# Performance work log

Hardware: AMD Instinct MI355X
Metric: run time of the kernel (lower is better)

Reference implementation:

```python
import jax, jax.numpy as jnp
import numpy as np

S, B, IN, H, DFF, OUT, L, NHEAD, WINDOW = 2048, 4, 64, 1024, 1024, 64, 3, 4, 4
EPS = 1e-5


def _layer_norm(x, scale, bias):
    m = jnp.mean(x, axis=-1, keepdims=True)
    v = jnp.var(x, axis=-1, keepdims=True)
    return (x - m) * jax.lax.rsqrt(v + EPS) * scale + bias


def setup_inputs() -> dict:
    key = jax.random.key(0)
    ks = jax.random.split(key, 12)
    s = 0.02
    return {
        "src": jax.random.normal(ks[0], (S, B, IN), dtype=jnp.float32),
        "Wenc": jax.random.normal(ks[1], (H, IN), dtype=jnp.float32) * s,
        "benc": jnp.zeros((H,), jnp.float32),
        "Wqkv": jax.random.normal(ks[2], (L, 3 * H, H), dtype=jnp.float32) * s,
        "bqkv": jnp.zeros((L, 3 * H), jnp.float32),
        "Wo": jax.random.normal(ks[3], (L, H, H), dtype=jnp.float32) * s,
        "bo": jnp.zeros((L, H), jnp.float32),
        "W1": jax.random.normal(ks[4], (L, DFF, H), dtype=jnp.float32) * s,
        "b1": jnp.zeros((L, DFF), jnp.float32),
        "W2": jax.random.normal(ks[5], (L, H, DFF), dtype=jnp.float32) * s,
        "b2": jnp.zeros((L, H), jnp.float32),
        "ln1_s": jnp.ones((L, H), jnp.float32),
        "ln1_b": jnp.zeros((L, H), jnp.float32),
        "ln2_s": jnp.ones((L, H), jnp.float32),
        "ln2_b": jnp.zeros((L, H), jnp.float32),
        "Wout": jax.random.normal(ks[6], (OUT, H), dtype=jnp.float32) * s,
        "bout": jnp.zeros((OUT,), jnp.float32),
    }


def _banded_mask(sz):
    # triu(1) masked + lower-band (j < i-4) masked => allowed: i-4 <= j <= i
    i = jnp.arange(sz)[:, None]
    j = jnp.arange(sz)[None, :]
    allowed = (j <= i) & (j >= i - WINDOW)
    return jnp.where(allowed, 0.0, -1e9).astype(jnp.float32)


def reference(src, Wenc, benc, Wqkv, bqkv, Wo, bo, W1, b1, W2, b2,
              ln1_s, ln1_b, ln2_s, ln2_b, Wout, bout):
    dh = H // NHEAD
    mask = _banded_mask(src.shape[0])  # [S, S]
    x = src @ Wenc.T + benc  # [S, B, H]  (NOTE: pos_encoder is never applied in the source)

    def layer(x, p):
        Wqkv_, bqkv_, Wo_, bo_, W1_, b1_, W2_, b2_, s1, g1, s2, g2 = p
        qkv = x @ Wqkv_.T + bqkv_  # [S, B, 3H]
        q, k, v = jnp.split(qkv, 3, axis=-1)
        sS, sB = x.shape[0], x.shape[1]
        q = q.reshape(sS, sB, NHEAD, dh)
        k = k.reshape(sS, sB, NHEAD, dh)
        v = v.reshape(sS, sB, NHEAD, dh)
        scores = jnp.einsum('sbhd,tbhd->bhst', q, k) / jnp.sqrt(jnp.float32(dh))
        scores = scores + mask  # broadcast over [b, h]
        attn = jax.nn.softmax(scores, axis=-1)
        ctx = jnp.einsum('bhst,tbhd->sbhd', attn, v).reshape(sS, sB, H)
        attn_out = ctx @ Wo_.T + bo_
        x = _layer_norm(x + attn_out, s1, g1)  # post-norm (PyTorch default)
        ff = jax.nn.relu(x @ W1_.T + b1_) @ W2_.T + b2_
        x = _layer_norm(x + ff, s2, g2)
        return x, None

    x, _ = jax.lax.scan(layer, x, (Wqkv, bqkv, Wo, bo, W1, b1, W2, b2,
                                   ln1_s, ln1_b, ln2_s, ln2_b))
    return x @ Wout.T + bout  # [S, B, OUT]
```

## Files before the change

kernel.cpp:

```cpp
#include <hip/hip_runtime.h>
#include <hip/hip_bf16.h>

#define S_LEN   2048
#define BATCH   4
#define IN_DIM  64
#define H_DIM   1024
#define DFF_DIM 1024
#define OUT_DIM 64
#define NLAYER  3
#define NHEADS  4
#define DHEAD   256
#define WIN     4
#define ROWS    (S_LEN*BATCH)
#define QKV_LD  (3*H_DIM)


typedef __bf16 bf16x8 __attribute__((ext_vector_type(8)));
typedef float  f32x4  __attribute__((ext_vector_type(4)));

__device__ __forceinline__ float bfbits2f(unsigned int u) {
  union { unsigned int i; float f; } c; c.i = u << 16; return c.f;
}
__device__ __forceinline__ unsigned short f2bfbits(float f) {
  __hip_bfloat16 h = __float2bfloat16(f);
  return __builtin_bit_cast(unsigned short, h);
}

__device__ __forceinline__ void g2l16(const void* g, void* l) {
  __builtin_amdgcn_global_load_lds((__attribute__((address_space(1))) void*)g,
                                   (__attribute__((address_space(3))) void*)l,
                                   16, 0, 0);
}

__global__ __launch_bounds__(256)
void cvt_k(const float* __restrict__ in, __hip_bfloat16* __restrict__ out, int n)
{
  int i = (blockIdx.x * 256 + threadIdx.x) * 4;
  if (i >= n) return;
  float4 v = *(const float4*)(in + i);
  uint2 o;
  o.x = (unsigned)f2bfbits(v.x) | ((unsigned)f2bfbits(v.y) << 16);
  o.y = (unsigned)f2bfbits(v.z) | ((unsigned)f2bfbits(v.w) << 16);
  *(uint2*)(out + i) = o;
}

template<int RELU, int OUTF32>
__global__ __launch_bounds__(256, 2)
void gemm_bt(const __hip_bfloat16* __restrict__ A, int lda,
             const __hip_bfloat16* __restrict__ B,
             const float* __restrict__ bias,
             void* __restrict__ Cp, int ldc,
             int M, int N, int K)
{
  __shared__ __align__(16) __hip_bfloat16 As[128 * 32];
  __shared__ __align__(16) __hip_bfloat16 Bs[128 * 32];

  const int tid  = threadIdx.x;
  const int lane = tid & 63;
  const int wave = tid >> 6;
  const int quad = lane >> 4;
  const int l16  = lane & 15;
  const int m0 = blockIdx.y * 128;
  const int n0 = blockIdx.x * 128;
  const int wr = (wave >> 1) * 64;
  const int wc = (wave & 1) * 64;

  const int p0  = wave * 64 + lane;
  const int p1  = p0 + 256;
  const int ar0 = p0 >> 2, ac0 = (((p0 & 3) ^ ((ar0 >> 1) & 3))) * 8;
  const int ar1 = p1 >> 2, ac1 = (((p1 & 3) ^ ((ar1 >> 1) & 3))) * 8;
  const int br0 = min(n0 + ar0, N - 1);
  const int br1 = min(n0 + ar1, N - 1);
  __hip_bfloat16* lA0 = &As[(wave * 64)       * 8];
  __hip_bfloat16* lA1 = &As[(wave * 64 + 256) * 8];
  __hip_bfloat16* lB0 = &Bs[(wave * 64)       * 8];
  __hip_bfloat16* lB1 = &Bs[(wave * 64 + 256) * 8];

  f32x4 acc[4][4] = {};

  for (int k0 = 0; k0 < K; k0 += 32) {
    g2l16(A + (size_t)(m0 + ar0) * lda + k0 + ac0, lA0);
    g2l16(A + (size_t)(m0 + ar1) * lda + k0 + ac1, lA1);
    g2l16(B + (size_t)br0 * K + k0 + ac0, lB0);
    g2l16(B + (size_t)br1 * K + k0 + ac1, lB1);
    __syncthreads();

    bf16x8 af[4], bfr[4];
#pragma unroll
    for (int i = 0; i < 4; i++) {
      const int row = wr + i * 16 + l16;
      af[i] = *(const bf16x8*)&As[row * 32 + ((quad ^ ((row >> 1) & 3)) * 8)];
    }
#pragma unroll
    for (int j = 0; j < 4; j++) {
      const int row = wc + j * 16 + l16;
      bfr[j] = *(const bf16x8*)&Bs[row * 32 + ((quad ^ ((row >> 1) & 3)) * 8)];
    }
#pragma unroll
    for (int i = 0; i < 4; i++)
#pragma unroll
      for (int j = 0; j < 4; j++)
        acc[i][j] = __builtin_amdgcn_mfma_f32_16x16x32_bf16(af[i], bfr[j], acc[i][j], 0, 0, 0);
    __syncthreads();
  }

#pragma unroll
  for (int j = 0; j < 4; j++) {
    int col = n0 + wc + j * 16 + l16;
    if (col < N) {
      float bv = bias[col];
#pragma unroll
      for (int i = 0; i < 4; i++) {
        int row = m0 + wr + i * 16 + quad * 4;
#pragma unroll
        for (int r = 0; r < 4; r++) {
          float v = acc[i][j][r] + bv;
          if (RELU) v = fmaxf(v, 0.f);
          if (OUTF32) ((float*)Cp)[(size_t)(row + r) * ldc + col] = v;
          else ((__hip_bfloat16*)Cp)[(size_t)(row + r) * ldc + col] = __float2bfloat16(v);
        }
      }
    }
  }
}

__global__ __launch_bounds__(256)
void attn_k(__hip_bfloat16* __restrict__ qkv)
{
  const int gw   = (blockIdx.x << 2) + (threadIdx.x >> 6);
  const int lane = threadIdx.x & 63;
  const int h = gw & (NHEADS - 1);
  const int b = (gw >> 2) & (BATCH - 1);
  const int s = gw >> 4;
  const size_t hoff = (size_t)h * DHEAD + (lane << 2);

  float q0, q1, q2, q3;
  {
    uint2 t = *(const uint2*)(qkv + (size_t)(s * BATCH + b) * QKV_LD + hoff);
    q0 = bfbits2f(t.x & 0xffff); q1 = bfbits2f(t.x >> 16);
    q2 = bfbits2f(t.y & 0xffff); q3 = bfbits2f(t.y >> 16);
  }

  float sc[WIN + 1];
#pragma unroll
  for (int jj = 0; jj <= WIN; jj++) {
    int j = s - WIN + jj;
    float v = -1e30f;
    if (j >= 0) {
      uint2 t = *(const uint2*)(qkv + (size_t)(j * BATCH + b) * QKV_LD + H_DIM + hoff);
      float p = q0 * bfbits2f(t.x & 0xffff) + q1 * bfbits2f(t.x >> 16)
              + q2 * bfbits2f(t.y & 0xffff) + q3 * bfbits2f(t.y >> 16);
#pragma unroll
      for (int o = 32; o; o >>= 1) p += __shfl_xor(p, o);
      v = p * 0.0625f;
    }
    sc[jj] = v;
  }

  float mx = sc[0];
#pragma unroll
  for (int jj = 1; jj <= WIN; jj++) mx = fmaxf(mx, sc[jj]);
  float p[WIN + 1], den = 0.f;
#pragma unroll
  for (int jj = 0; jj <= WIN; jj++) { p[jj] = __expf(sc[jj] - mx); den += p[jj]; }

  float a0 = 0.f, a1 = 0.f, a2 = 0.f, a3 = 0.f;
#pragma unroll
  for (int jj = 0; jj <= WIN; jj++) {
    int j = s - WIN + jj;
    if (j >= 0) {
      uint2 t = *(const uint2*)(qkv + (size_t)(j * BATCH + b) * QKV_LD + 2 * H_DIM + hoff);
      a0 += p[jj] * bfbits2f(t.x & 0xffff); a1 += p[jj] * bfbits2f(t.x >> 16);
      a2 += p[jj] * bfbits2f(t.y & 0xffff); a3 += p[jj] * bfbits2f(t.y >> 16);
    }
  }
  float rl = 1.f / den;
  uint2 o;
  o.x = (unsigned)f2bfbits(a0 * rl) | ((unsigned)f2bfbits(a1 * rl) << 16);
  o.y = (unsigned)f2bfbits(a2 * rl) | ((unsigned)f2bfbits(a3 * rl) << 16);
  *(uint2*)(qkv + (size_t)(s * BATCH + b) * QKV_LD + hoff) = o;
}

__global__ __launch_bounds__(256)
void add_ln_k(__hip_bfloat16* __restrict__ x, const __hip_bfloat16* __restrict__ y, int ys,
              const float* __restrict__ g, const float* __restrict__ be)
{
  const int row = blockIdx.x, tid = threadIdx.x;
  const size_t base = (size_t)row * H_DIM + tid * 4;
  uint2 xv = *(const uint2*)(x + base);
  uint2 yv = *(const uint2*)(y + (size_t)row * ys + tid * 4);
  float t0 = bfbits2f(xv.x & 0xffff) + bfbits2f(yv.x & 0xffff);
  float t1 = bfbits2f(xv.x >> 16)    + bfbits2f(yv.x >> 16);
  float t2 = bfbits2f(xv.y & 0xffff) + bfbits2f(yv.y & 0xffff);
  float t3 = bfbits2f(xv.y >> 16)    + bfbits2f(yv.y >> 16);
  float s  = t0 + t1 + t2 + t3;
  float ss = t0 * t0 + t1 * t1 + t2 * t2 + t3 * t3;
#pragma unroll
  for (int o = 32; o; o >>= 1) { s += __shfl_down(s, o); ss += __shfl_down(ss, o); }
  __shared__ float rs[4], rss[4];
  if ((tid & 63) == 0) { rs[tid >> 6] = s; rss[tid >> 6] = ss; }
  __syncthreads();
  float S  = rs[0] + rs[1] + rs[2] + rs[3];
  float SS = rss[0] + rss[1] + rss[2] + rss[3];
  const float inv = 1.f / (float)H_DIM;
  float mean = S * inv;
  float var  = SS * inv - mean * mean;
  float rstd = rsqrtf(var + 1e-5f);
  float4 gv = *(const float4*)(g + tid * 4);
  float4 bv = *(const float4*)(be + tid * 4);
  float o0 = (t0 - mean) * rstd * gv.x + bv.x;
  float o1 = (t1 - mean) * rstd * gv.y + bv.y;
  float o2 = (t2 - mean) * rstd * gv.z + bv.z;
  float o3 = (t3 - mean) * rstd * gv.w + bv.w;
  uint2 ob;
  ob.x = (unsigned)f2bfbits(o0) | ((unsigned)f2bfbits(o1) << 16);
  ob.y = (unsigned)f2bfbits(o2) | ((unsigned)f2bfbits(o3) << 16);
  *(uint2*)(x + base) = ob;
}

extern "C" void kernel_launch(void* const* d_in, const int* in_sizes, int n_in,
                              void* d_out, int out_size, void* d_ws, size_t ws_size,
                              hipStream_t stream) {
  const float* src   = (const float*)d_in[0];
  const float* Wenc  = (const float*)d_in[1];
  const float* benc  = (const float*)d_in[2];
  const float* Wqkv  = (const float*)d_in[3];
  const float* bqkv  = (const float*)d_in[4];
  const float* Wo    = (const float*)d_in[5];
  const float* bo    = (const float*)d_in[6];
  const float* W1    = (const float*)d_in[7];
  const float* b1    = (const float*)d_in[8];
  const float* W2    = (const float*)d_in[9];
  const float* b2    = (const float*)d_in[10];
  const float* ln1s  = (const float*)d_in[11];
  const float* ln1b  = (const float*)d_in[12];
  const float* ln2s  = (const float*)d_in[13];
  const float* ln2b  = (const float*)d_in[14];
  const float* Wout  = (const float*)d_in[15];
  const float* bout  = (const float*)d_in[16];

  char* ws = (char*)d_ws;
  __hip_bfloat16* WB   = (__hip_bfloat16*)ws;
  __hip_bfloat16* srcb = WB;
  __hip_bfloat16* wenc = WB + 524288;
  __hip_bfloat16* wqkv = WB + 589824;
  __hip_bfloat16* wo   = WB + 10027008;
  __hip_bfloat16* w1   = WB + 13172736;
  __hip_bfloat16* w2   = WB + 16318464;
  __hip_bfloat16* wout = WB + 19464192;
  __hip_bfloat16* xb  = (__hip_bfloat16*)(ws + (size_t)40 * 1048576);
  __hip_bfloat16* qkv = (__hip_bfloat16*)(ws + (size_t)56 * 1048576);
  __hip_bfloat16* ctxp = qkv;
  __hip_bfloat16* ybuf = qkv + H_DIM;
  __hip_bfloat16* hbuf = qkv + 2 * H_DIM;

  const dim3 blk(256);
  #define CVT(inp, outp, n) cvt_k<<<dim3(((n) / 4 + 255) / 256), blk, 0, stream>>>(inp, outp, n)

  CVT(src,  srcb, 524288);
  CVT(Wenc, wenc, 65536);
  CVT(Wqkv, wqkv, 9437184);
  CVT(Wo,   wo,   3145728);
  CVT(W1,   w1,   3145728);
  CVT(W2,   w2,   3145728);
  CVT(Wout, wout, 65536);

  gemm_bt<0, 0><<<dim3(H_DIM / 128, ROWS / 128), blk, 0, stream>>>(
      srcb, IN_DIM, wenc, benc, xb, H_DIM, ROWS, H_DIM, IN_DIM);

  for (int l = 0; l < NLAYER; l++) {
    gemm_bt<0, 0><<<dim3(QKV_LD / 128, ROWS / 128), blk, 0, stream>>>(
        xb, H_DIM, wqkv + (size_t)l * QKV_LD * H_DIM, bqkv + l * QKV_LD,
        qkv, QKV_LD, ROWS, QKV_LD, H_DIM);
    attn_k<<<dim3(ROWS * NHEADS / 4), blk, 0, stream>>>(qkv);
    gemm_bt<0, 0><<<dim3(H_DIM / 128, ROWS / 128), blk, 0, stream>>>(
        ctxp, QKV_LD, wo + (size_t)l * H_DIM * H_DIM, bo + l * H_DIM,
        ybuf, QKV_LD, ROWS, H_DIM, H_DIM);
    add_ln_k<<<dim3(ROWS), blk, 0, stream>>>(xb, ybuf, QKV_LD, ln1s + l * H_DIM, ln1b + l * H_DIM);
    gemm_bt<1, 0><<<dim3(DFF_DIM / 128, ROWS / 128), blk, 0, stream>>>(
        xb, H_DIM, w1 + (size_t)l * DFF_DIM * H_DIM, b1 + l * DFF_DIM,
        hbuf, QKV_LD, ROWS, DFF_DIM, H_DIM);
    gemm_bt<0, 0><<<dim3(H_DIM / 128, ROWS / 128), blk, 0, stream>>>(
        hbuf, QKV_LD, w2 + (size_t)l * H_DIM * DFF_DIM, b2 + l * H_DIM,
        ybuf, QKV_LD, ROWS, H_DIM, DFF_DIM);
    add_ln_k<<<dim3(ROWS), blk, 0, stream>>>(xb, ybuf, QKV_LD, ln2s + l * H_DIM, ln2b + l * H_DIM);
  }

  gemm_bt<0, 1><<<dim3(1, ROWS / 128), blk, 0, stream>>>(
      xb, H_DIM, wout, bout, d_out, OUT_DIM, ROWS, OUT_DIM, H_DIM);
}
```

Baseline: 797.1 us.

## Double-buffer LDS tiles in bf16 GEMM to overlap loads with MFMA

Splits the A and B shared-memory tiles into two buffers. The loads for the next K-slice are issued right after the barrier, while MFMAs run on the current slice, and the trailing barrier per iteration is removed. The goal is to hide global-to-LDS load latency behind compute in every projection and FFN GEMM. In exchange, shared memory per block doubles to 32KB, which could affect occupancy, and correctness now relies on the barrier also waiting for the pending async loads.

```diff
diff --git a/kernel.cpp b/kernel.cpp
--- a/kernel.cpp
+++ b/kernel.cpp
@@ -52,8 +52,8 @@
              void* __restrict__ Cp, int ldc,
              int M, int N, int K)
 {
-  __shared__ __align__(16) __hip_bfloat16 As[128 * 32];
-  __shared__ __align__(16) __hip_bfloat16 Bs[128 * 32];
+  __shared__ __align__(16) __hip_bfloat16 As[2][128 * 32];
+  __shared__ __align__(16) __hip_bfloat16 Bs[2][128 * 32];
 
   const int tid  = threadIdx.x;
   const int lane = tid & 63;
@@ -71,37 +71,49 @@
   const int ar1 = p1 >> 2, ac1 = (((p1 & 3) ^ ((ar1 >> 1) & 3))) * 8;
   const int br0 = min(n0 + ar0, N - 1);
   const int br1 = min(n0 + ar1, N - 1);
-  __hip_bfloat16* lA0 = &As[(wave * 64)       * 8];
-  __hip_bfloat16* lA1 = &As[(wave * 64 + 256) * 8];
-  __hip_bfloat16* lB0 = &Bs[(wave * 64)       * 8];
-  __hip_bfloat16* lB1 = &Bs[(wave * 64 + 256) * 8];
+  const int lo0 = (wave * 64)       * 8;
+  const int lo1 = (wave * 64 + 256) * 8;
+
+  const __hip_bfloat16* gA0 = A + (size_t)(m0 + ar0) * lda + ac0;
+  const __hip_bfloat16* gA1 = A + (size_t)(m0 + ar1) * lda + ac1;
+  const __hip_bfloat16* gB0 = B + (size_t)br0 * K + ac0;
+  const __hip_bfloat16* gB1 = B + (size_t)br1 * K + ac1;
 
   f32x4 acc[4][4] = {};
-
-  for (int k0 = 0; k0 < K; k0 += 32) {
-    g2l16(A + (size_t)(m0 + ar0) * lda + k0 + ac0, lA0);
-    g2l16(A + (size_t)(m0 + ar1) * lda + k0 + ac1, lA1);
-    g2l16(B + (size_t)br0 * K + k0 + ac0, lB0);
-    g2l16(B + (size_t)br1 * K + k0 + ac1, lB1);
+  const int nk = K >> 5;
+
+  g2l16(gA0, &As[0][lo0]);
+  g2l16(gA1, &As[0][lo1]);
+  g2l16(gB0, &Bs[0][lo0]);
+  g2l16(gB1, &Bs[0][lo1]);
+
+  for (int t = 0; t < nk; ++t) {
+    const int cur = t & 1, nxt = cur ^ 1;
     __syncthreads();
+    if (t + 1 < nk) {
+      const int k = (t + 1) << 5;
+      g2l16(gA0 + k, &As[nxt][lo0]);
+      g2l16(gA1 + k, &As[nxt][lo1]);
+      g2l16(gB0 + k, &Bs[nxt][lo0]);
+      g2l16(gB1 + k, &Bs[nxt][lo1]);
+    }
 
     bf16x8 af[4], bfr[4];
 #pragma unroll
     for (int i = 0; i < 4; i++) {
       const int row = wr + i * 16 + l16;
-      af[i] = *(const bf16x8*)&As[row * 32 + ((quad ^ ((row >> 1) & 3)) * 8)];
+      af[i] = *(const bf16x8*)&As[cur][row * 32 + ((quad ^ ((row >> 1) & 3)) * 8)];
     }
 #pragma unroll
     for (int j = 0; j < 4; j++) {
       const int row = wc + j * 16 + l16;
-      bfr[j] = *(const bf16x8*)&Bs[row * 32 + ((quad ^ ((row >> 1) & 3)) * 8)];
+      bfr[j] = *(const bf16x8*)&Bs[cur][row * 32 + ((quad ^ ((row >> 1) & 3)) * 8)];
     }
 #pragma unroll
     for (int i = 0; i < 4; i++)
 #pragma unroll
       for (int j = 0; j < 4; j++)
         acc[i][j] = __builtin_amdgcn_mfma_f32_16x16x32_bf16(af[i], bfr[j], acc[i][j], 0, 0, 0);
-    __syncthreads();
   }
 
 #pragma unroll
```

New measurement: 798.2 us. About the same (+0.1%).
